# Kernel optimization log

Hardware: AMD Instinct MI355X
Metric: run time of the kernel (lower is better)

## Reference

```python
import jax, jax.numpy as jnp
import numpy as np

IN_DIM = 512
OUT_DIM = 512
GRID_SIZE = 5
SPLINE_ORDER = 3
N_COEFFS = GRID_SIZE + SPLINE_ORDER            # 8
N_KNOTS = GRID_SIZE + 2 * SPLINE_ORDER + 1     # 12
BATCH = 16384


def setup_inputs() -> dict:
    key = jax.random.key(0)
    k0, k1, k2 = jax.random.split(key, 3)
    step = 2.0 / GRID_SIZE
    x = jax.random.normal(k0, (BATCH, IN_DIM), dtype=jnp.float32)
    coeffs = jax.random.normal(k1, (OUT_DIM, IN_DIM * N_COEFFS), dtype=jnp.float32) * 0.1
    bound = 1.0 / np.sqrt(IN_DIM)  # kaiming_uniform with a=sqrt(5) for a Linear-like weight
    base_weight = jax.random.uniform(k2, (OUT_DIM, IN_DIM), minval=-bound, maxval=bound, dtype=jnp.float32)
    grid_steps_log = jnp.full((IN_DIM, N_KNOTS - 1), np.log(step), dtype=jnp.float32)
    grid_start = jnp.full((IN_DIM, 1), -1.0 - step * SPLINE_ORDER, dtype=jnp.float32)
    res_scale = jnp.zeros((1,), dtype=jnp.float32)
    return {"x": x, "coeffs": coeffs, "base_weight": base_weight,
            "grid_steps_log": grid_steps_log, "grid_start": grid_start,
            "res_scale": res_scale}


def _get_grid(grid_steps_log, grid_start):
    steps = jax.nn.softplus(grid_steps_log)            # (in, n_knots-1)
    offsets = jnp.cumsum(steps, axis=1)
    return jnp.concatenate([grid_start, grid_start + offsets], axis=1)  # (in, n_knots)


def _b_spline(x, grid):
    # x: (B, in), grid: (in, n_knots) -> bases: (B, in, n_coeffs)
    xe = x[..., None]                                   # (B, in, 1)
    left = grid[:, :-1]
    right = grid[:, 1:]
    bases = ((xe >= left) & (xe < right)).astype(x.dtype)  # (B, in, n_knots-1)
    eps = 1e-8
    denom = right - left                                # (in, n_knots-1)
    for k in range(SPLINE_ORDER):
        left_num = xe - grid[:, :-(2 + k)]              # (B, in, m-1)
        right_num = grid[:, 2 + k:] - xe
        l = left_num / (denom[:, :-(1 + k)] + eps)
        r = right_num / (denom[:, 1 + k:] + eps)
        bases = l * bases[:, :, :-1] + r * bases[:, :, 1:]
    return bases                                        # (B, in, n_coeffs)


def reference(x, coeffs, base_weight, grid_steps_log, grid_start, res_scale):
    grid = _get_grid(grid_steps_log, grid_start)
    spline_basis = _b_spline(x, grid)                   # (B, in, n_coeffs)
    B = spline_basis.shape[0]
    spline_flat = spline_basis.reshape(B, -1)           # (B, in*n_coeffs), in-major
    spline_out = spline_flat @ coeffs.T                 # (B, out)
    base_out = jax.nn.silu(x) @ base_weight.T           # (B, out)
    y = spline_out + base_out + res_scale * x           # residual (in_dim == out_dim)
    return jnp.tanh(y)
```

## Files before the change

kernel.cpp:

```cpp
#include <hip/hip_runtime.h>
#include <stdint.h>
#include <stddef.h>


typedef __attribute__((ext_vector_type(8))) _Float16 half8;
typedef __attribute__((ext_vector_type(4))) float f32x4;

#define IN_DIM   512
#define OUT_DIM  512
#define BATCH    16384
#define KCH      576

__device__ __forceinline__ unsigned pk2(float a, float b) {
  _Float16 ha = (_Float16)a, hb = (_Float16)b;
  unsigned short ua = __builtin_bit_cast(unsigned short, ha);
  unsigned short ub = __builtin_bit_cast(unsigned short, hb);
  return (unsigned)ua | ((unsigned)ub << 16);
}
__device__ __forceinline__ uint4 pk8(float4 a, float4 b) {
  uint4 r;
  r.x = pk2(a.x, a.y); r.y = pk2(a.z, a.w);
  r.z = pk2(b.x, b.y); r.w = pk2(b.z, b.w);
  return r;
}

__device__ __forceinline__ uint4 basis8(float xv, float g0, float rh) {
  float u  = (xv - g0) * rh;
  float tf = floorf(u);
  float f  = u - tf;
  int   t  = (int)tf;
  bool valid = (u >= 0.f) && (u < 11.f);
  t = min(max(t, 0), 10);
  float f2 = f * f, f3 = f2 * f;
  float omf = 1.f - f;
  float v0 = omf * omf * omf;
  float v1 = fmaf(f2, fmaf(3.f, f, -6.f), 4.f);
  float v2 = fmaf(f, fmaf(f, fmaf(-3.f, f, 3.f), 3.f), 1.f);
  float v3 = f3;
  uint64_t pack = ((uint64_t)pk2(v2, v3) << 32) | (uint64_t)pk2(v0, v1);
  pack = valid ? pack : 0ull;
  const int base = 48 - 16 * t;
  uint4 r;
  uint32_t* rp = (uint32_t*)&r;
  #pragma unroll
  for (int i = 0; i < 4; ++i) {
    int amt = base + 32 * i;
    uint32_t lo = (amt >= 0 && amt < 64) ? (uint32_t)(pack >> amt) : 0u;
    uint32_t hi = (amt < 0 && amt > -64) ? (uint32_t)(pack << (-amt)) : 0u;
    rp[i] = lo | hi;
  }
  return r;
}

__global__ __launch_bounds__(256) void kan_prep(
    const float* __restrict__ x,
    const float* __restrict__ coeffs,
    const float* __restrict__ bwt,
    const float* __restrict__ gsl,
    const float* __restrict__ gstart,
    uint4* __restrict__ A16,
    uint4* __restrict__ B16)
{
  int id   = blockIdx.x * 256 + threadIdx.x;
  int row  = id / KCH;
  int slot = id - row * KCH;

  if (row < BATCH) {
    uint4 v;
    if (slot < 512) {
      float gl = gsl[slot * 11];
      float h  = fmaxf(gl, 0.f) + log1pf(expf(-fabsf(gl)));
      v = basis8(x[(size_t)row * IN_DIM + slot], gstart[slot], 1.f / h);
    } else {
      const float* xs = x + (size_t)row * IN_DIM + (slot - 512) * 8;
      float4 a = *(const float4*)xs, b = *(const float4*)(xs + 4);
      float f[8] = {a.x, a.y, a.z, a.w, b.x, b.y, b.z, b.w};
      #pragma unroll
      for (int j = 0; j < 8; ++j) f[j] = f[j] / (1.f + __expf(-f[j]));
      v.x = pk2(f[0], f[1]); v.y = pk2(f[2], f[3]);
      v.z = pk2(f[4], f[5]); v.w = pk2(f[6], f[7]);
    }
    int sw = (slot & ~3) | (((slot & 3) + ((row >> 1) & 3)) & 3);
    A16[(size_t)row * KCH + sw] = v;
  } else {
    int n = row - BATCH;
    const float* s = (slot < 512)
        ? coeffs + (size_t)n * 4096 + slot * 8
        : bwt    + (size_t)n * 512  + (slot - 512) * 8;
    float4 a = *(const float4*)s, b = *(const float4*)(s + 4);
    uint4 v = pk8(a, b);
    int sw = (slot & ~3) | (((slot & 3) + ((n >> 1) & 3)) & 3);
    B16[(size_t)n * KCH + sw] = v;
  }
}

__device__ __forceinline__ void gload_lds16(const uint4* g, uint4* l) {
  __builtin_amdgcn_global_load_lds(
      (const __attribute__((address_space(1))) void*)g,
      (__attribute__((address_space(3))) void*)l, 16, 0, 0);
}

__global__ __launch_bounds__(256, 2) void kan_gemm(
    const uint4* __restrict__ A16,
    const uint4* __restrict__ B16,
    const float* __restrict__ x,
    const float* __restrict__ rsc,
    float* __restrict__ out)
{
  __shared__ uint4 As[512];
  __shared__ uint4 Bs[512];

  const int tid  = threadIdx.x;
  const int lane = tid & 63;
  const int wv   = tid >> 6;
  const int row0 = blockIdx.y << 7;
  const int n0   = blockIdx.x << 7;

  const int q    = lane >> 4;
  const int l15  = lane & 15;
  const int wrow = (wv >> 1) << 6;
  const int wcol = (wv & 1) << 6;
  const int cq   = (q + ((l15 >> 1) & 3)) & 3;

  const int s0 = wv * 128 + lane;
  const int s1 = s0 + 64;
  const uint4* ga0 = A16 + (size_t)(row0 + (s0 >> 2)) * KCH + (s0 & 3);
  const uint4* ga1 = A16 + (size_t)(row0 + (s1 >> 2)) * KCH + (s1 & 3);
  const uint4* gb0 = B16 + (size_t)(n0  + (s0 >> 2)) * KCH + (s0 & 3);
  const uint4* gb1 = B16 + (size_t)(n0  + (s1 >> 2)) * KCH + (s1 & 3);
  uint4* la0 = &As[wv * 128];
  uint4* la1 = &As[wv * 128 + 64];
  uint4* lb0 = &Bs[wv * 128];
  uint4* lb1 = &Bs[wv * 128 + 64];

  f32x4 acc[4][4];
  #pragma unroll
  for (int a = 0; a < 4; ++a)
    #pragma unroll
    for (int b = 0; b < 4; ++b)
      acc[a][b] = (f32x4){0.f, 0.f, 0.f, 0.f};

  for (int kt = 0; kt < 144; ++kt) {
    gload_lds16(ga0, la0);
    gload_lds16(ga1, la1);
    gload_lds16(gb0, lb0);
    gload_lds16(gb1, lb1);
    ga0 += 4; ga1 += 4; gb0 += 4; gb1 += 4;
    __syncthreads();

    half8 af[4], bg[4];
    #pragma unroll
    for (int tm = 0; tm < 4; ++tm)
      af[tm] = *(const half8*)&As[(wrow + tm * 16 + l15) * 4 + cq];
    #pragma unroll
    for (int tn = 0; tn < 4; ++tn)
      bg[tn] = *(const half8*)&Bs[(wcol + tn * 16 + l15) * 4 + cq];
    #pragma unroll
    for (int tm = 0; tm < 4; ++tm)
      #pragma unroll
      for (int tn = 0; tn < 4; ++tn)
        acc[tm][tn] = __builtin_amdgcn_mfma_f32_16x16x32_f16(
            af[tm], bg[tn], acc[tm][tn], 0, 0, 0);
    __syncthreads();
  }

  const float rs = rsc[0];
  #pragma unroll
  for (int tm = 0; tm < 4; ++tm) {
    #pragma unroll
    for (int tn = 0; tn < 4; ++tn) {
      #pragma unroll
      for (int r = 0; r < 4; ++r) {
        int m = row0 + wrow + tm * 16 + q * 4 + r;
        int n = n0 + wcol + tn * 16 + l15;
        float xv = x[(size_t)m * IN_DIM + n];
        float y  = acc[tm][tn][r] + rs * xv;
        float e  = __expf(-2.f * fabsf(y));
        float t  = copysignf((1.f - e) / (1.f + e), y);
        out[(size_t)m * OUT_DIM + n] = t;
      }
    }
  }
}

__device__ __forceinline__ int swz(int r, int c) {
  return r * 4 + ((c + (r >> 1)) & 3);
}

__global__ __launch_bounds__(256, 2) void kan_main(
    const float* __restrict__ x, const float* __restrict__ coeffs,
    const float* __restrict__ bwt, const float* __restrict__ gsl,
    const float* __restrict__ gstart, const float* __restrict__ rsc,
    float* __restrict__ out)
{
  __shared__ uint4 At[512];
  __shared__ uint4 Bt[512];
  __shared__ float2 Cs[512];

  const int tid  = threadIdx.x;
  const int lane = tid & 63;
  const int wv   = tid >> 6;
  const int row0 = blockIdx.y << 7;
  const int n0   = blockIdx.x << 7;

  const int q    = lane >> 4;
  const int l15  = lane & 15;
  const int wrow = (wv >> 1) << 6;
  const int wcol = (wv & 1) << 6;

  for (int d = tid; d < IN_DIM; d += 256) {
    float v  = gsl[d * 11];
    float sp = fmaxf(v, 0.f) + log1pf(expf(-fabsf(v)));
    Cs[d] = make_float2(gstart[d], 1.f / sp);
  }
  __syncthreads();

  f32x4 acc[4][4];
  #pragma unroll
  for (int a = 0; a < 4; ++a)
    #pragma unroll
    for (int b = 0; b < 4; ++b)
      acc[a][b] = (f32x4){0.f, 0.f, 0.f, 0.f};

  const int br0 = tid >> 2,        bc0 = tid & 3;
  const int br1 = (tid + 256) >> 2, bc1 = tid & 3;

  auto do_mfma = [&]() {
    half8 af[4], bg[4];
    #pragma unroll
    for (int tm = 0; tm < 4; ++tm) {
      int m = wrow + tm * 16 + l15;
      af[tm] = *(const half8*)&At[swz(m, q)];
    }
    #pragma unroll
    for (int tn = 0; tn < 4; ++tn) {
      int n = wcol + tn * 16 + l15;
      bg[tn] = *(const half8*)&Bt[swz(n, q)];
    }
    #pragma unroll
    for (int tm = 0; tm < 4; ++tm)
      #pragma unroll
      for (int tn = 0; tn < 4; ++tn)
        acc[tm][tn] = __builtin_amdgcn_mfma_f32_16x16x32_f16(
            af[tm], bg[tn], acc[tm][tn], 0, 0, 0);
  };

  const float* bp0 = coeffs + (size_t)(n0 + br0) * 4096 + 1024 * bc0;
  const float* bp1 = coeffs + (size_t)(n0 + br1) * 4096 + 1024 * bc1;
  const float* xp0 = x + (size_t)(row0 + lane) * IN_DIM + 128 * wv;
  const float* xp1 = xp0 + (size_t)64 * IN_DIM;

  for (int kt4 = 0; kt4 < 32; ++kt4) {
    float4 xa = *(const float4*)(xp0 + kt4 * 4);
    float4 xb = *(const float4*)(xp1 + kt4 * 4);
    float xr0[4] = {xa.x, xa.y, xa.z, xa.w};
    float xr1[4] = {xb.x, xb.y, xb.z, xb.w};
    #pragma unroll
    for (int j = 0; j < 4; ++j) {
      const int kt = kt4 * 4 + j;
      const float* s0 = bp0 + kt * 8;
      const float* s1 = bp1 + kt * 8;
      float4 b0a = *(const float4*)(s0), b0b = *(const float4*)(s0 + 4);
      float4 b1a = *(const float4*)(s1), b1b = *(const float4*)(s1 + 4);

      float2 c = Cs[128 * wv + kt];
      uint4 p0 = basis8(xr0[j], c.x, c.y);
      uint4 p1 = basis8(xr1[j], c.x, c.y);

      Bt[swz(br0, bc0)] = pk8(b0a, b0b);
      Bt[swz(br1, bc1)] = pk8(b1a, b1b);
      At[swz(lane, wv)]      = p0;
      At[swz(lane + 64, wv)] = p1;
      __syncthreads();
      do_mfma();
      __syncthreads();
    }
  }

  for (int kt = 0; kt < 16; ++kt) {
    const int k0 = kt * 32;
    const float* s0 = bwt + (size_t)(n0 + br0) * 512 + k0 + bc0 * 8;
    const float* s1 = bwt + (size_t)(n0 + br1) * 512 + k0 + bc1 * 8;
    float4 b0a = *(const float4*)(s0), b0b = *(const float4*)(s0 + 4);
    float4 b1a = *(const float4*)(s1), b1b = *(const float4*)(s1 + 4);

    uint4 p[2];
    #pragma unroll
    for (int rr = 0; rr < 2; ++rr) {
      int idx = tid + rr * 256;
      int r = idx >> 2, cch = idx & 3;
      const float* xs = x + (size_t)(row0 + r) * IN_DIM + k0 + cch * 8;
      float4 xc = *(const float4*)(xs), xd = *(const float4*)(xs + 4);
      float f[8] = {xc.x, xc.y, xc.z, xc.w, xd.x, xd.y, xd.z, xd.w};
      #pragma unroll
      for (int jj = 0; jj < 8; ++jj) f[jj] = f[jj] / (1.f + __expf(-f[jj]));
      p[rr].x = pk2(f[0], f[1]); p[rr].y = pk2(f[2], f[3]);
      p[rr].z = pk2(f[4], f[5]); p[rr].w = pk2(f[6], f[7]);
    }

    Bt[swz(br0, bc0)] = pk8(b0a, b0b);
    Bt[swz(br1, bc1)] = pk8(b1a, b1b);
    #pragma unroll
    for (int rr = 0; rr < 2; ++rr) {
      int idx = tid + rr * 256;
      At[swz(idx >> 2, idx & 3)] = p[rr];
    }
    __syncthreads();
    do_mfma();
    __syncthreads();
  }

  const float rs = rsc[0];
  #pragma unroll
  for (int tm = 0; tm < 4; ++tm) {
    #pragma unroll
    for (int tn = 0; tn < 4; ++tn) {
      #pragma unroll
      for (int r = 0; r < 4; ++r) {
        int m = row0 + wrow + tm * 16 + q * 4 + r;
        int n = n0 + wcol + tn * 16 + l15;
        float xv = x[(size_t)m * IN_DIM + n];
        float y  = acc[tm][tn][r] + rs * xv;
        float e  = __expf(-2.f * fabsf(y));
        float t  = copysignf((1.f - e) / (1.f + e), y);
        out[(size_t)m * OUT_DIM + n] = t;
      }
    }
  }
}

extern "C" void kernel_launch(void* const* d_in, const int* in_sizes, int n_in,
                              void* d_out, int out_size, void* d_ws, size_t ws_size,
                              hipStream_t stream) {
  const float* x      = (const float*)d_in[0];
  const float* coeffs = (const float*)d_in[1];
  const float* bwt    = (const float*)d_in[2];
  const float* gsl    = (const float*)d_in[3];
  const float* gstart = (const float*)d_in[4];
  const float* rsc    = (const float*)d_in[5];
  float* out = (float*)d_out;
  (void)in_sizes; (void)n_in; (void)out_size;

  const size_t needA = (size_t)BATCH * KCH * 16;
  const size_t needB = (size_t)OUT_DIM * KCH * 16;

  if (d_ws != nullptr && ws_size >= needA + needB) {
    uint4* A16 = (uint4*)d_ws;
    uint4* B16 = (uint4*)((char*)d_ws + needA);
    const int prep_blocks = ((BATCH + OUT_DIM) * KCH) / 256;
    hipLaunchKernelGGL(kan_prep, dim3(prep_blocks), dim3(256), 0, stream,
                       x, coeffs, bwt, gsl, gstart, A16, B16);
    hipLaunchKernelGGL(kan_gemm, dim3(4, 128), dim3(256), 0, stream,
                       (const uint4*)A16, (const uint4*)B16, x, rsc, out);
  } else {
    hipLaunchKernelGGL(kan_main, dim3(4, 128), dim3(256), 0, stream,
                       x, coeffs, bwt, gsl, gstart, rsc, out);
  }
}
```

Measured before the change: 238.3 us.

## Double-buffer GEMM LDS tiles, remap blocks for L2 locality, precompute grid constants

The GEMM main loop now uses two LDS buffers, so the global-to-LDS load of the next K-slice is issued before the MFMA work on the current slice, and there is one barrier per step instead of two. Workgroups move to a 1D grid with an XCD-aware remapping so that blocks sharing A rows run close together, which is meant to improve cache reuse. The per-column softplus and reciprocal grid constants are computed once in a tiny new kernel instead of being recomputed for every batch row in prep. The cost is a third kernel launch and doubled LDS use, which may lower occupancy.

```diff
diff --git a/kernel.cpp b/kernel.cpp
--- a/kernel.cpp
+++ b/kernel.cpp
@@ -52,12 +52,23 @@
   return r;
 }
 
+__global__ __launch_bounds__(256) void kan_consts(
+    const float* __restrict__ gsl, const float* __restrict__ gstart,
+    float2* __restrict__ cst)
+{
+  int d = blockIdx.x * 256 + threadIdx.x;
+  if (d < IN_DIM) {
+    float v  = gsl[d * 11];
+    float sp = fmaxf(v, 0.f) + log1pf(expf(-fabsf(v)));
+    cst[d] = make_float2(gstart[d], 1.f / sp);
+  }
+}
+
 __global__ __launch_bounds__(256) void kan_prep(
     const float* __restrict__ x,
     const float* __restrict__ coeffs,
     const float* __restrict__ bwt,
-    const float* __restrict__ gsl,
-    const float* __restrict__ gstart,
+    const float2* __restrict__ cst,
     uint4* __restrict__ A16,
     uint4* __restrict__ B16)
 {
@@ -68,9 +79,8 @@
   if (row < BATCH) {
     uint4 v;
     if (slot < 512) {
-      float gl = gsl[slot * 11];
-      float h  = fmaxf(gl, 0.f) + log1pf(expf(-fabsf(gl)));
-      v = basis8(x[(size_t)row * IN_DIM + slot], gstart[slot], 1.f / h);
+      float2 c = cst[slot];
+      v = basis8(x[(size_t)row * IN_DIM + slot], c.x, c.y);
     } else {
       const float* xs = x + (size_t)row * IN_DIM + (slot - 512) * 8;
       float4 a = *(const float4*)xs, b = *(const float4*)(xs + 4);
@@ -107,14 +117,17 @@
     const float* __restrict__ rsc,
     float* __restrict__ out)
 {
-  __shared__ uint4 As[512];
-  __shared__ uint4 Bs[512];
+  __shared__ uint4 As[2][512];
+  __shared__ uint4 Bs[2][512];
 
   const int tid  = threadIdx.x;
   const int lane = tid & 63;
   const int wv   = tid >> 6;
-  const int row0 = blockIdx.y << 7;
-  const int n0   = blockIdx.x << 7;
+
+  const int bid  = blockIdx.x;
+  const int wg   = ((bid & 7) << 6) | (bid >> 3);
+  const int row0 = (wg >> 2) << 7;
+  const int n0   = (wg & 3) << 7;
 
   const int q    = lane >> 4;
   const int l15  = lane & 15;
@@ -128,10 +141,6 @@
   const uint4* ga1 = A16 + (size_t)(row0 + (s1 >> 2)) * KCH + (s1 & 3);
   const uint4* gb0 = B16 + (size_t)(n0  + (s0 >> 2)) * KCH + (s0 & 3);
   const uint4* gb1 = B16 + (size_t)(n0  + (s1 >> 2)) * KCH + (s1 & 3);
-  uint4* la0 = &As[wv * 128];
-  uint4* la1 = &As[wv * 128 + 64];
-  uint4* lb0 = &Bs[wv * 128];
-  uint4* lb1 = &Bs[wv * 128 + 64];
 
   f32x4 acc[4][4];
   #pragma unroll
@@ -140,29 +149,43 @@
     for (int b = 0; b < 4; ++b)
       acc[a][b] = (f32x4){0.f, 0.f, 0.f, 0.f};
 
-  for (int kt = 0; kt < 144; ++kt) {
-    gload_lds16(ga0, la0);
-    gload_lds16(ga1, la1);
-    gload_lds16(gb0, lb0);
-    gload_lds16(gb1, lb1);
-    ga0 += 4; ga1 += 4; gb0 += 4; gb1 += 4;
-    __syncthreads();
-
+  auto stage = [&](int b, int kt) {
+    const int o = kt * 4;
+    gload_lds16(ga0 + o, &As[b][wv * 128]);
+    gload_lds16(ga1 + o, &As[b][wv * 128 + 64]);
+    gload_lds16(gb0 + o, &Bs[b][wv * 128]);
+    gload_lds16(gb1 + o, &Bs[b][wv * 128 + 64]);
+  };
+  auto compute = [&](int b) {
     half8 af[4], bg[4];
     #pragma unroll
     for (int tm = 0; tm < 4; ++tm)
-      af[tm] = *(const half8*)&As[(wrow + tm * 16 + l15) * 4 + cq];
+      af[tm] = *(const half8*)&As[b][(wrow + tm * 16 + l15) * 4 + cq];
     #pragma unroll
     for (int tn = 0; tn < 4; ++tn)
-      bg[tn] = *(const half8*)&Bs[(wcol + tn * 16 + l15) * 4 + cq];
+      bg[tn] = *(const half8*)&Bs[b][(wcol + tn * 16 + l15) * 4 + cq];
     #pragma unroll
     for (int tm = 0; tm < 4; ++tm)
       #pragma unroll
       for (int tn = 0; tn < 4; ++tn)
         acc[tm][tn] = __builtin_amdgcn_mfma_f32_16x16x32_f16(
             af[tm], bg[tn], acc[tm][tn], 0, 0, 0);
+  };
+
+  stage(0, 0);
+  __syncthreads();
+  for (int kt = 0; kt < 142; kt += 2) {
+    stage(1, kt + 1);
+    compute(0);
     __syncthreads();
-  }
+    stage(0, kt + 2);
+    compute(1);
+    __syncthreads();
+  }
+  stage(1, 143);
+  compute(0);
+  __syncthreads();
+  compute(1);
 
   const float rs = rsc[0];
   #pragma unroll
@@ -343,14 +366,18 @@
 
   const size_t needA = (size_t)BATCH * KCH * 16;
   const size_t needB = (size_t)OUT_DIM * KCH * 16;
-
-  if (d_ws != nullptr && ws_size >= needA + needB) {
-    uint4* A16 = (uint4*)d_ws;
-    uint4* B16 = (uint4*)((char*)d_ws + needA);
+  const size_t needC = (size_t)IN_DIM * 8;
+
+  if (d_ws != nullptr && ws_size >= needA + needB + needC) {
+    uint4*  A16 = (uint4*)d_ws;
+    uint4*  B16 = (uint4*)((char*)d_ws + needA);
+    float2* cst = (float2*)((char*)d_ws + needA + needB);
+    hipLaunchKernelGGL(kan_consts, dim3(2), dim3(256), 0, stream,
+                       gsl, gstart, cst);
     const int prep_blocks = ((BATCH + OUT_DIM) * KCH) / 256;
     hipLaunchKernelGGL(kan_prep, dim3(prep_blocks), dim3(256), 0, stream,
-                       x, coeffs, bwt, gsl, gstart, A16, B16);
-    hipLaunchKernelGGL(kan_gemm, dim3(4, 128), dim3(256), 0, stream,
+                       x, coeffs, bwt, (const float2*)cst, A16, B16);
+    hipLaunchKernelGGL(kan_gemm, dim3(512), dim3(256), 0, stream,
                        (const uint4*)A16, (const uint4*)B16, x, rsc, out);
   } else {
     hipLaunchKernelGGL(kan_main, dim3(4, 128), dim3(256), 0, stream,
```

Result: no change. 240.0 us (+0.7%).
